# Kernel optimization log

Hardware: AMD Instinct MI355X
Metric: run time of the kernel (lower is better)

## Reference

```python
import jax, jax.numpy as jnp
import numpy as np
from jax import lax

B, T = 128, 512
V, D = 100000, 100   # word vocab, word embedding dim
H = 100              # per-direction LSTM hidden (concat -> 200)
L = 25               # number of CRF labels


def setup_inputs() -> dict:
    key = jax.random.key(0)
    ks = jax.random.split(key, 16)
    s = 0.02
    inp = {
        "tok_tensor": jax.random.randint(ks[0], (B, T), 0, V, dtype=jnp.int32),
        "tag_tensor": jax.random.randint(ks[1], (B, T), 0, L, dtype=jnp.int32),
        "lengths": jnp.full((B,), T, dtype=jnp.int32),
        "word_emb": jax.random.normal(ks[2], (V, D), jnp.float32) * s,
        # forward-direction LSTM (PyTorch gate order i,f,g,o)
        "w_ih_f": jax.random.normal(ks[3], (4 * H, D), jnp.float32) * s,
        "w_hh_f": jax.random.normal(ks[4], (4 * H, H), jnp.float32) * s,
        "b_ih_f": jax.random.normal(ks[5], (4 * H,), jnp.float32) * s,
        "b_hh_f": jax.random.normal(ks[6], (4 * H,), jnp.float32) * s,
        # backward-direction LSTM
        "w_ih_b": jax.random.normal(ks[7], (4 * H, D), jnp.float32) * s,
        "w_hh_b": jax.random.normal(ks[8], (4 * H, H), jnp.float32) * s,
        "b_ih_b": jax.random.normal(ks[9], (4 * H,), jnp.float32) * s,
        "b_hh_b": jax.random.normal(ks[10], (4 * H,), jnp.float32) * s,
        # hidden2tag linear
        "w_tag": jax.random.normal(ks[11], (L, 2 * H), jnp.float32) * s,
        "b_tag": jax.random.normal(ks[12], (L,), jnp.float32) * s,
        # CRF params
        "transitions": jax.random.normal(ks[13], (L, L), jnp.float32) * 0.1,
        "start_trans": jax.random.normal(ks[14], (L,), jnp.float32) * 0.1,
        "end_trans": jax.random.normal(ks[15], (L,), jnp.float32) * 0.1,
    }
    return inp


def _lstm(x_tbd, w_ih, w_hh, b_ih, b_hh, reverse):
    """x_tbd: [T,B,D] -> hidden states [T,B,H], aligned with input time axis."""
    Bh = x_tbd.shape[1]
    Hh = w_hh.shape[1]
    h0 = jnp.zeros((Bh, Hh), x_tbd.dtype)
    c0 = jnp.zeros((Bh, Hh), x_tbd.dtype)

    def step(carry, xt):
        h, c = carry
        gates = xt @ w_ih.T + b_ih + h @ w_hh.T + b_hh
        i, f, g, o = jnp.split(gates, 4, axis=-1)
        i = jax.nn.sigmoid(i); f = jax.nn.sigmoid(f)
        g = jnp.tanh(g); o = jax.nn.sigmoid(o)
        c = f * c + i * g
        h = o * jnp.tanh(c)
        return (h, c), h

    _, hs = lax.scan(step, (h0, c0), x_tbd, reverse=reverse)
    return hs


def _crf_nll(emissions, tags, mask, transitions, start_trans, end_trans):
    """Sum over batch of -(gold path score - log partition).
    emissions: [B,T,L], tags: [B,T] int, mask: [B,T] float (1=valid)."""
    Bb = emissions.shape[0]
    b_idx = jnp.arange(Bb)
    em_t = emissions.transpose(1, 0, 2)   # [T,B,L]
    tags_t = tags.T                       # [T,B]
    mask_t = mask.T                       # [T,B]

    # --- gold path score ---
    first_tags = tags_t[0]
    score0 = start_trans[first_tags] + em_t[0][b_idx, first_tags]

    def num_step(score, inp):
        em, tp, tc, m = inp  # emissions[t], tags[t-1], tags[t], mask[t]
        s = transitions[tp, tc] + em[b_idx, tc]
        return score + m * s, None

    gold, _ = lax.scan(num_step, score0,
                       (em_t[1:], tags_t[:-1], tags_t[1:], mask_t[1:]))
    last_idx = jnp.sum(mask, axis=1).astype(jnp.int32) - 1
    last_tags = tags[b_idx, last_idx]
    gold = gold + end_trans[last_tags]

    # --- log partition (forward algorithm) ---
    alpha0 = start_trans + em_t[0]  # [B,L]

    def part_step(alpha, inp):
        em, m = inp
        # [B,L_prev,1] + [L_prev,L_next] + [B,1,L_next]
        nxt = jax.nn.logsumexp(alpha[:, :, None] + transitions[None] + em[:, None, :], axis=1)
        alpha = jnp.where(m[:, None] > 0, nxt, alpha)
        return alpha, None

    alpha, _ = lax.scan(part_step, alpha0, (em_t[1:], mask_t[1:]))
    logZ = jax.nn.logsumexp(alpha + end_trans, axis=1)
    return jnp.sum(logZ - gold)


def reference(tok_tensor, tag_tensor, lengths,
              word_emb, w_ih_f, w_hh_f, b_ih_f, b_hh_f,
              w_ih_b, w_hh_b, b_ih_b, b_hh_b,
              w_tag, b_tag, transitions, start_trans, end_trans):
    # word embedding lookup: [B,T,D]
    tok_embs = word_emb[tok_tensor]
    x_tbd = tok_embs.transpose(1, 0, 2)  # [T,B,D]
    # BiLSTM encoder (dropout off: eval / deterministic reference)
    h_fwd = _lstm(x_tbd, w_ih_f, w_hh_f, b_ih_f, b_hh_f, reverse=False)
    h_bwd = _lstm(x_tbd, w_ih_b, w_hh_b, b_ih_b, b_hh_b, reverse=True)
    seq = jnp.concatenate([h_fwd, h_bwd], axis=-1).transpose(1, 0, 2)  # [B,T,2H]
    # hidden2tag
    emissions = jnp.einsum('btd,ld->btl', seq, w_tag) + b_tag  # [B,T,L]
    # CRF negative log-likelihood
    mask = (jnp.arange(T)[None, :] < lengths[:, None]).astype(emissions.dtype)
    return _crf_nll(emissions, tag_tensor, mask, transitions, start_trans, end_trans)
```

## Files before the change

### kernel.cpp

```cpp
#include <hip/hip_runtime.h>
#include <cstdint>
#include <cstddef>

#define BB 128
#define TT 512
#define DD 100
#define HH 100
#define NG 400
#define LL 25
#define TS 32
#define NTILE 16
#define F_LOG2E 1.44269504088896340736f
#define F_LN2   0.69314718055994530942f

typedef __decltype(__builtin_amdgcn_cvt_pkrtz(0.f, 0.f)) h2_t;
typedef _Float16 v8h __attribute__((ext_vector_type(8)));
typedef float v4f __attribute__((ext_vector_type(4)));

__device__ __forceinline__ h2_t bc_h2(unsigned int u) {
  return __builtin_bit_cast(h2_t, u);
}
__device__ __forceinline__ unsigned int pk(float x, float y) {
  return __builtin_bit_cast(unsigned int, __builtin_amdgcn_cvt_pkrtz(x, y));
}

__device__ __forceinline__ float fdot2(h2_t a, h2_t b, float c) {
#if __has_builtin(__builtin_amdgcn_fdot2)
  return __builtin_amdgcn_fdot2(a, b, c, false);
#else
  return c + (float)a[0] * (float)b[0] + (float)a[1] * (float)b[1];
#endif
}

__device__ __forceinline__ float fexp2(float x) { return __builtin_amdgcn_exp2f(x); }
__device__ __forceinline__ float flog2(float x) { return __builtin_amdgcn_logf(x); }
__device__ __forceinline__ float frcp(float x)  { return __builtin_amdgcn_rcpf(x); }

__device__ __forceinline__ float sigmoid_f(float x) {
  return frcp(1.f + fexp2(-F_LOG2E * x));
}
__device__ __forceinline__ float tanh_f(float x) {
  float e = fexp2(2.f * F_LOG2E * x);
  return 1.f - 2.f * frcp(e + 1.f);
}

template <int CTRL>
__device__ __forceinline__ float qadd(float v) {
#if __has_builtin(__builtin_amdgcn_mov_dpp)
  int m = __builtin_amdgcn_mov_dpp(__builtin_bit_cast(int, v), CTRL, 0xF, 0xF, true);
  return v + __builtin_bit_cast(float, m);
#else
  int x = (CTRL == 177) ? 1 : 2;
  return v + __shfl_xor(v, x);
#endif
}

template <int CTRL>
__device__ __forceinline__ float qperm(float v) {
#if __has_builtin(__builtin_amdgcn_mov_dpp)
  int m = __builtin_amdgcn_mov_dpp(__builtin_bit_cast(int, v), CTRL, 0xF, 0xF, true);
  return __builtin_bit_cast(float, m);
#else
  int x = (CTRL == 177) ? 1 : 2;
  return __shfl_xor(v, x);
#endif
}

__device__ __forceinline__ float rfl(float v) {
  return __builtin_bit_cast(float,
      __builtin_amdgcn_readfirstlane(__builtin_bit_cast(int, v)));
}

__device__ __forceinline__ void wave_fence() {
#if __has_builtin(__builtin_amdgcn_wave_barrier)
  __builtin_amdgcn_wave_barrier();
#endif
}

__device__ __forceinline__ void lds_barrier() {
  __builtin_amdgcn_s_waitcnt(0xC07F);
  __builtin_amdgcn_s_barrier();
}

__global__ __launch_bounds__(512, 1) void lstm_fused6(
    const int* __restrict__ tok, const float* __restrict__ emb,
    const float* __restrict__ w_ih_f, const float* __restrict__ w_ih_b,
    const float* __restrict__ b_ih_f, const float* __restrict__ b_hh_f,
    const float* __restrict__ b_ih_b, const float* __restrict__ b_hh_b,
    const float* __restrict__ w_hh_f, const float* __restrict__ w_hh_b,
    const float* __restrict__ w_tag, const float* __restrict__ b_tag,
    float* __restrict__ em_f, float* __restrict__ em_b)
{
  const int tid = threadIdx.x;
  const int b   = blockIdx.x & 127;
  const int dir = blockIdx.x >> 7;
  const float* w_hh = dir ? w_hh_b : w_hh_f;
  const float* w_ih = dir ? w_ih_b : w_ih_f;
  const float* b_ih = dir ? b_ih_b : b_ih_f;
  const float* b_hh = dir ? b_hh_b : b_hh_f;
  float* emo = dir ? em_b : em_f;

  __shared__ __align__(16) unsigned short gin_lds[TS * 400];
  __shared__ __align__(16) unsigned int xlds[TS * 68];
  __shared__ __align__(16) unsigned int hhist[TS * 68];
  __shared__ __align__(16) unsigned int hls0[56];
  __shared__ __align__(16) unsigned int hls1[56];

  const int wv   = tid >> 6;
  const int lane = tid & 63;
  const int l16  = lane & 15;
  const int quad = lane >> 4;
  const int c0b  = (25 * wv) >> 3;
  const int c1b  = (25 * (wv + 1)) >> 3;
  const int ncol = c1b - c0b;

  v8h bfr[4][4];
  int pcol[4];
#pragma unroll
  for (int ci = 0; ci < 4; ++ci) {
    const int cc = (ci < ncol) ? (c0b + ci) : c0b;
    const int n  = 16 * cc + l16;
    const float* wr = w_ih + (size_t)n * DD;
#pragma unroll
    for (int f = 0; f < 3; ++f) {
      const float* wp = wr + f * 32 + quad * 8;
      float4 va = *(const float4*)(wp);
      float4 vb = *(const float4*)(wp + 4);
      uint4 u;
      u.x = pk(va.x, va.y); u.y = pk(va.z, va.w);
      u.z = pk(vb.x, vb.y); u.w = pk(vb.z, vb.w);
      bfr[ci][f] = __builtin_bit_cast(v8h, u);
    }
    {
      uint4 u = {0u, 0u, 0u, 0u};
      if (quad == 0) {
        float4 va = *(const float4*)(wr + 96);
        u.x = pk(va.x, va.y); u.y = pk(va.z, va.w);
      }
      bfr[ci][3] = __builtin_bit_cast(v8h, u);
    }
    const int qn = (n * 41) >> 12;
    pcol[ci] = ((n - 100 * qn) << 2) + qn;
  }

  for (int i = tid; i < TS * 18; i += 512) {
    int row = i / 18;
    int d = i - row * 18;
    xlds[row * 68 + 50 + d] = 0u;
    hhist[row * 68 + 50 + d] = 0u;
  }

  const int jl = lane >> 2;
  const int gp = (lane >> 1) & 1;
  const int s2 = lane & 1;
  const int j  = 8 * jl + wv;
  const bool uact  = (jl < 12) || (jl == 12 && wv < 4);
  const int  goff  = 8 * j + 4 * gp;
  const int  hidx  = j + (j >= 50 ? 6 : 0);

  h2_t wA[25], wB[25];
  float biasA = 0.f, biasB = 0.f;
  if (uact) {
    const int g0 = 2 * gp, g1 = 2 * gp + 1;
    const float* rA = w_hh + (size_t)(g0 * 100 + j) * HH + 50 * s2;
    const float* rB = w_hh + (size_t)(g1 * 100 + j) * HH + 50 * s2;
#pragma unroll
    for (int d = 0; d < 25; ++d) {
      float2 vA = *(const float2*)(rA + 2 * d);
      float2 vB = *(const float2*)(rB + 2 * d);
      wA[d] = __builtin_amdgcn_cvt_pkrtz(vA.x, vA.y);
      wB[d] = __builtin_amdgcn_cvt_pkrtz(vB.x, vB.y);
    }
    biasA = b_ih[g0 * 100 + j] + b_hh[g0 * 100 + j];
    biasB = b_ih[g1 * 100 + j] + b_hh[g1 * 100 + j];
  }
  const float kkA = gp ? (2.f * F_LOG2E) : (-F_LOG2E);
  const float cAA = gp ? -2.f : 1.f;
  const float cBA = gp ? 1.f : 0.f;

  const int ew    = wv - 4;
  const int ecb   = ew & 1;
  const int erg   = (ew >> 1) & 1;
  const int encol = 16 * ecb + l16;
  const bool eact2 = (wv >= 4) && (encol < LL);
  v8h etag[4];
  float ebias = 0.f;
  if (wv >= 4) {
#pragma unroll
    for (int f = 0; f < 3; ++f) {
      uint4 u = {0u, 0u, 0u, 0u};
      if (eact2) {
        const float* wp = w_tag + (size_t)encol * 200 + dir * 100 + f * 32 + quad * 8;
        float4 va = *(const float4*)(wp);
        float4 vb = *(const float4*)(wp + 4);
        u.x = pk(va.x, va.y); u.y = pk(va.z, va.w);
        u.z = pk(vb.x, vb.y); u.w = pk(vb.z, vb.w);
      }
      etag[f] = __builtin_bit_cast(v8h, u);
    }
    {
      uint4 u = {0u, 0u, 0u, 0u};
      if (eact2 && quad == 0) {
        float4 va = *(const float4*)(w_tag + (size_t)encol * 200 + dir * 100 + 96);
        u.x = pk(va.x, va.y); u.y = pk(va.z, va.w);
      }
      etag[3] = __builtin_bit_cast(v8h, u);
    }
    if (eact2 && dir == 0) ebias = b_tag[encol];
  }

  if (tid < 56) { hls0[tid] = 0u; hls1[tid] = 0u; }

  const int tprow = tid / 13;
  const int tps   = tid - 13 * tprow;
  const bool tp_act = tid < 416;

  float4 xa = {0, 0, 0, 0}, xb = {0, 0, 0, 0};
  if (tp_act) {
    int ii = tprow;
    int tt = dir ? (TT - 1 - ii) : ii;
    int tk = tok[b * TT + tt];
    const float* xp = emb + (size_t)tk * DD + 8 * tps;
    xa = *(const float4*)xp;
    if (tps < 12) xb = *(const float4*)(xp + 4);
  }

  float c = 0.f;
  unsigned int gnext = 0u;

#define SD2(d, hw) { h2_t hv = bc_h2(hw);                                  \
  pA = fdot2(wA[d], hv, pA); pB = fdot2(wB[d], hv, pB); }

#define SCAN2(HRD, HWR, ROW)                                               \
  {                                                                        \
    if (uact) {                                                            \
      unsigned int gcurr = gnext;                                          \
      int nr = ((ROW) < TS - 1) ? (ROW) + 1 : TS - 1;                      \
      gnext = *(const unsigned int*)((const char*)gin_lds + nr * 800 + goff); \
      const unsigned int* hp = (HRD) + 28 * s2;                            \
      uint4 u0 = *((const uint4*)hp);                                      \
      uint4 u1 = *((const uint4*)(hp + 4));                                \
      uint4 u2 = *((const uint4*)(hp + 8));                                \
      uint4 u3 = *((const uint4*)(hp + 12));                               \
      uint4 u4 = *((const uint4*)(hp + 16));                               \
      uint4 u5 = *((const uint4*)(hp + 20));                               \
      unsigned int u6 = hp[24];                                            \
      float pA = 0.f, pB = 0.f;                                            \
      SD2(0, u0.x)  SD2(1, u0.y)  SD2(2, u0.z)  SD2(3, u0.w)               \
      SD2(4, u1.x)  SD2(5, u1.y)  SD2(6, u1.z)  SD2(7, u1.w)               \
      SD2(8, u2.x)  SD2(9, u2.y)  SD2(10, u2.z) SD2(11, u2.w)              \
      SD2(12, u3.x) SD2(13, u3.y) SD2(14, u3.z) SD2(15, u3.w)              \
      SD2(16, u4.x) SD2(17, u4.y) SD2(18, u4.z) SD2(19, u4.w)              \
      SD2(20, u5.x) SD2(21, u5.y) SD2(22, u5.z) SD2(23, u5.w)              \
      SD2(24, u6)                                                          \
      pA = qadd<177>(pA); pB = qadd<177>(pB);                              \
      h2_t gx = bc_h2(gcurr);                                              \
      float gA = pA + biasA + (float)gx[0];                                \
      float gB = pB + biasB + (float)gx[1];                                \
      float yA = fexp2(kkA * gA);                                          \
      float rA_ = frcp(1.f + yA);                                          \
      float actA = fmaf(cAA, rA_, cBA);                                    \
      float actB = sigmoid_f(gB);                                          \
      float othA = qperm<78>(actA);                                        \
      float othB = qperm<78>(actB);                                        \
      float prod = actA * othA;                                            \
      float fsel = gp ? othB : actB;                                       \
      float osel = gp ? actB : othB;                                       \
      c = fmaf(fsel, c, prod);                                             \
      float hvv = osel * tanh_f(c);                                        \
      if ((lane & 3) == 0) {                                               \
        __fp16 hh = (__fp16)hvv;                                           \
        ((__fp16*)(HWR))[hidx] = hh;                                       \
        ((__fp16*)hhist)[(ROW) * 136 + j] = hh;                            \
      }                                                                    \
    }                                                                      \
    lds_barrier();                                                         \
  }

#define EMIT_GEMM(TB)                                                      \
  {                                                                        \
    const unsigned int* hb = hhist + (erg * 16 + l16) * 68 + quad * 4;     \
    v8h ah0 = __builtin_bit_cast(v8h, *(const uint4*)(hb));                \
    v8h ah1 = __builtin_bit_cast(v8h, *(const uint4*)(hb + 16));           \
    v8h ah2 = __builtin_bit_cast(v8h, *(const uint4*)(hb + 32));           \
    v8h ah3 = __builtin_bit_cast(v8h, *(const uint4*)(hb + 48));           \
    v4f ea = {0.f, 0.f, 0.f, 0.f};                                         \
    ea = __builtin_amdgcn_mfma_f32_16x16x32_f16(ah0, etag[0], ea, 0, 0, 0);\
    ea = __builtin_amdgcn_mfma_f32_16x16x32_f16(ah1, etag[1], ea, 0, 0, 0);\
    ea = __builtin_amdgcn_mfma_f32_16x16x32_f16(ah2, etag[2], ea, 0, 0, 0);\
    ea = __builtin_amdgcn_mfma_f32_16x16x32_f16(ah3, etag[3], ea, 0, 0, 0);\
    if (eact2) {                                                           \
      const int tb = (TB) + erg * 16 + quad * 4;                           \
      _Pragma("unroll")                                                    \
      for (int r = 0; r < 4; ++r) {                                        \
        int t = dir ? (TT - 1 - (tb + r)) : (tb + r);                      \
        emo[((size_t)b * TT + t) * LL + encol] = ea[r] + ebias;            \
      }                                                                    \
    }                                                                      \
  }

  __syncthreads();

  for (int T = 0; T < NTILE; ++T) {
    if (tp_act) {
      unsigned int* xr = xlds + tprow * 68 + 4 * tps;
      if (tps < 12) {
        uint4 u;
        u.x = pk(xa.x, xa.y); u.y = pk(xa.z, xa.w);
        u.z = pk(xb.x, xb.y); u.w = pk(xb.z, xb.w);
        *(uint4*)xr = u;
      } else {
        xr[0] = pk(xa.x, xa.y);
        xr[1] = pk(xa.z, xa.w);
      }
    }
    __syncthreads();

    {
      v8h af[2][4];
#pragma unroll
      for (int rg = 0; rg < 2; ++rg)
#pragma unroll
        for (int f = 0; f < 4; ++f)
          af[rg][f] = __builtin_bit_cast(v8h,
              *(const uint4*)(xlds + (rg * 16 + l16) * 68 + f * 16 + quad * 4));

      if (tp_act && T + 1 < NTILE) {
        int ii = (T + 1) * TS + tprow;
        int tt = dir ? (TT - 1 - ii) : ii;
        int tk = tok[b * TT + tt];
        const float* xp = emb + (size_t)tk * DD + 8 * tps;
        xa = *(const float4*)xp;
        if (tps < 12) xb = *(const float4*)(xp + 4);
      }

      __fp16* gout = (__fp16*)gin_lds;
#pragma unroll
      for (int ci = 0; ci < 4; ++ci) {
        if (ci >= ncol) break;
        const int p = pcol[ci];
#pragma unroll
        for (int rg = 0; rg < 2; ++rg) {
          v4f acc = {0.f, 0.f, 0.f, 0.f};
          acc = __builtin_amdgcn_mfma_f32_16x16x32_f16(af[rg][0], bfr[ci][0], acc, 0, 0, 0);
          acc = __builtin_amdgcn_mfma_f32_16x16x32_f16(af[rg][1], bfr[ci][1], acc, 0, 0, 0);
          acc = __builtin_amdgcn_mfma_f32_16x16x32_f16(af[rg][2], bfr[ci][2], acc, 0, 0, 0);
          acc = __builtin_amdgcn_mfma_f32_16x16x32_f16(af[rg][3], bfr[ci][3], acc, 0, 0, 0);
          const int rowb = rg * 16 + quad * 4;
#pragma unroll
          for (int r = 0; r < 4; ++r)
            gout[(rowb + r) * 400 + p] = (__fp16)acc[r];
        }
      }

      if (wv >= 4 && T > 0) {
        EMIT_GEMM((T - 1) * TS)
      }
    }
    __syncthreads();
    if (uact) gnext = *(const unsigned int*)((const char*)gin_lds + goff);

    for (int it = 0; it < TS; it += 2) {
      SCAN2(hls0, hls1, it)
      SCAN2(hls1, hls0, it + 1)
    }
  }

  if (wv >= 4) {
    EMIT_GEMM((NTILE - 1) * TS)
  }
#undef EMIT_GEMM
#undef SCAN2
#undef SD2
}

#define CHN  8
#define CLEN 64
__device__ __align__(16) float g_PT[(size_t)BB * CHN * LL * 28];

__global__ __launch_bounds__(128, 2) void crf_chunks(
    const float* __restrict__ em_f, const float* __restrict__ em_b,
    const float* __restrict__ trans)
{
  const int tid = threadIdx.x;
  const int b   = blockIdx.x >> 3;
  const int c   = blockIdx.x & 7;
  const int ts  = c * CLEN;

  __shared__ __align__(16) float Al[2][LL][28];
  __shared__ __align__(16) float el[CLEN][32];

  {
    const int row  = tid >> 1;
    const int half = tid & 1;
    const int jb   = half ? 13 : 0;
    const int nj   = half ? 12 : 13;
    const float* pf = em_f + ((size_t)b * TT + ts + row) * LL;
    const float* pb = em_b + ((size_t)b * TT + ts + row) * LL;
    for (int q = 0; q < nj; ++q) {
      int jj = jb + q;
      el[row][jj] = fexp2((pf[jj] + pb[jj]) * F_LOG2E);
    }
  }

  const bool lact = tid < 125;
  const int i  = tid / 5;
  const int jg = tid - 5 * i;
  const int j0 = 5 * jg;

  float E[25][5];
  if (lact) {
#pragma unroll
    for (int k = 0; k < 25; ++k) {
      const float* tr = trans + k * 25 + j0;
#pragma unroll
      for (int u = 0; u < 5; ++u)
        E[k][u] = fexp2(tr[u] * F_LOG2E - 5.f);
    }
#pragma unroll
    for (int u = 0; u < 5; ++u)
      Al[0][i][j0 + u] = (i == j0 + u) ? 1.f : 0.f;
  }
  __syncthreads();

  int p = 0;
  const int s0 = (c == 0) ? 1 : 0;
  for (int st = s0; st < CLEN; ++st) {
    if (lact) {
      const float* ar = &Al[p][i][0];
      float4 q0 = *(const float4*)(ar);
      float4 q1 = *(const float4*)(ar + 4);
      float4 q2 = *(const float4*)(ar + 8);
      float4 q3 = *(const float4*)(ar + 12);
      float4 q4 = *(const float4*)(ar + 16);
      float4 q5 = *(const float4*)(ar + 20);
      float a24 = ar[24];
      float e0 = el[st][j0];
      float e1 = el[st][j0 + 1];
      float e2 = el[st][j0 + 2];
      float e3 = el[st][j0 + 3];
      float e4 = el[st][j0 + 4];
      float av[25] = {q0.x, q0.y, q0.z, q0.w, q1.x, q1.y, q1.z, q1.w,
                      q2.x, q2.y, q2.z, q2.w, q3.x, q3.y, q3.z, q3.w,
                      q4.x, q4.y, q4.z, q4.w, q5.x, q5.y, q5.z, q5.w, a24};
      float c0 = 0.f, c1 = 0.f, c2 = 0.f, c3 = 0.f, c4 = 0.f;
#pragma unroll
      for (int k = 0; k < 25; ++k) {
        float avk = av[k];
        c0 = fmaf(avk, E[k][0], c0);
        c1 = fmaf(avk, E[k][1], c1);
        c2 = fmaf(avk, E[k][2], c2);
        c3 = fmaf(avk, E[k][3], c3);
        c4 = fmaf(avk, E[k][4], c4);
      }
      float* wr = &Al[p ^ 1][i][j0];
      wr[0] = c0 * e0; wr[1] = c1 * e1; wr[2] = c2 * e2;
      wr[3] = c3 * e3; wr[4] = c4 * e4;
    }
    __syncthreads();
    p ^= 1;
  }

  if (lact) {
    const size_t base = ((size_t)(b * CHN + c)) * LL;
#pragma unroll
    for (int u = 0; u < 5; ++u)
      g_PT[(base + (j0 + u)) * 28 + i] = Al[p][i][j0 + u];
  }
}

__global__ __launch_bounds__(128) void crf_combine(
    const float* __restrict__ em_f, const float* __restrict__ em_b,
    const int* __restrict__ tags, const int* __restrict__ lengths,
    const float* __restrict__ trans,
    const float* __restrict__ startt, const float* __restrict__ endt,
    float* __restrict__ out)
{
  const int tid = threadIdx.x;
  const int b   = blockIdx.x;

  __shared__ __align__(16) float Vs[28];

  if (tid < 64) {
    const int lane = tid;
    const int j = (lane < LL) ? lane : 0;
    const float* ef0 = em_f + (size_t)b * TT * LL;
    const float* eb0 = em_b + (size_t)b * TT * LL;
    float v = fexp2((startt[j] + ef0[j] + eb0[j]) * F_LOG2E);
    float C = 0.f;
    for (int c = 0; c < CHN; ++c) {
      if (lane < LL) Vs[lane] = v;
      wave_fence();
      float4 s0 = *(const float4*)(Vs);
      float4 s1 = *(const float4*)(Vs + 4);
      float4 s2 = *(const float4*)(Vs + 8);
      float4 s3 = *(const float4*)(Vs + 12);
      float4 s4 = *(const float4*)(Vs + 16);
      float4 s5 = *(const float4*)(Vs + 20);
      float s24 = Vs[24];
      wave_fence();
      const float* pr = g_PT + ((size_t)(b * CHN + c) * LL + j) * 28;
      float4 p0 = *(const float4*)(pr);
      float4 p1 = *(const float4*)(pr + 4);
      float4 p2 = *(const float4*)(pr + 8);
      float4 p3 = *(const float4*)(pr + 12);
      float4 p4 = *(const float4*)(pr + 16);
      float4 p5 = *(const float4*)(pr + 20);
      float p24 = pr[24];
      float nv = s0.x * p0.x;
      nv = fmaf(s0.y, p0.y, nv); nv = fmaf(s0.z, p0.z, nv); nv = fmaf(s0.w, p0.w, nv);
      nv = fmaf(s1.x, p1.x, nv); nv = fmaf(s1.y, p1.y, nv);
      nv = fmaf(s1.z, p1.z, nv); nv = fmaf(s1.w, p1.w, nv);
      nv = fmaf(s2.x, p2.x, nv); nv = fmaf(s2.y, p2.y, nv);
      nv = fmaf(s2.z, p2.z, nv); nv = fmaf(s2.w, p2.w, nv);
      nv = fmaf(s3.x, p3.x, nv); nv = fmaf(s3.y, p3.y, nv);
      nv = fmaf(s3.z, p3.z, nv); nv = fmaf(s3.w, p3.w, nv);
      nv = fmaf(s4.x, p4.x, nv); nv = fmaf(s4.y, p4.y, nv);
      nv = fmaf(s4.z, p4.z, nv); nv = fmaf(s4.w, p4.w, nv);
      nv = fmaf(s5.x, p5.x, nv); nv = fmaf(s5.y, p5.y, nv);
      nv = fmaf(s5.z, p5.z, nv); nv = fmaf(s5.w, p5.w, nv);
      nv = fmaf(s24, p24, nv);
      float nv0 = rfl(nv);
      int k = ((__builtin_bit_cast(int, nv0) >> 23) & 255) - 127;
      k = (k > 100) ? 100 : ((k < -100) ? -100 : k);
      float scl = __builtin_bit_cast(float, (127 - k) << 23);
      v = nv * scl;
      C += (float)k;
    }
    float term = (lane < LL) ? v * fexp2(endt[j] * F_LOG2E) : 0.f;
    for (int o = 32; o > 0; o >>= 1) term += __shfl_down(term, o);
    if (lane == 0)
      atomicAdd(out, (flog2(term) + C + 5.f * 511.f) * F_LN2);
  } else {
    const int lane = tid & 63;
    const int len = lengths[b];
    float acc = 0.f;
#pragma unroll
    for (int k = 0; k < 8; ++k) {
      int t = k * 64 + lane;
      int tg = tags[b * TT + t];
      size_t ei = ((size_t)b * TT + t) * LL + tg;
      float e = em_f[ei] + em_b[ei];
      float term;
      if (t == 0) term = startt[tg] + e;
      else        term = trans[tags[b * TT + t - 1] * LL + tg] + e;
      if (t == len - 1) term += endt[tg];
      if (t < len) acc += term;
    }
    for (int o = 32; o > 0; o >>= 1) acc += __shfl_down(acc, o);
    if (lane == 0) atomicAdd(out, -acc);
  }
}

extern "C" void kernel_launch(void* const* d_in, const int* in_sizes, int n_in,
                              void* d_out, int out_size, void* d_ws, size_t ws_size,
                              hipStream_t stream) {
  const int*   tok   = (const int*)d_in[0];
  const int*   tags  = (const int*)d_in[1];
  const int*   lens  = (const int*)d_in[2];
  const float* emb   = (const float*)d_in[3];
  const float* wif   = (const float*)d_in[4];
  const float* whf   = (const float*)d_in[5];
  const float* bif   = (const float*)d_in[6];
  const float* bhf   = (const float*)d_in[7];
  const float* wib   = (const float*)d_in[8];
  const float* whb   = (const float*)d_in[9];
  const float* bib   = (const float*)d_in[10];
  const float* bhb   = (const float*)d_in[11];
  const float* wtag  = (const float*)d_in[12];
  const float* btag  = (const float*)d_in[13];
  const float* trans = (const float*)d_in[14];
  const float* st    = (const float*)d_in[15];
  const float* en    = (const float*)d_in[16];

  char* wsb = (char*)d_ws;
  float* em_f = (float*)wsb;
  float* em_b = (float*)(wsb + 6553600);

  hipMemsetAsync(d_out, 0, sizeof(float), stream);

  lstm_fused6<<<256, 512, 0, stream>>>(tok, emb, wif, wib, bif, bhf, bib, bhb,
                                       whf, whb, wtag, btag, em_f, em_b);
  crf_chunks<<<BB * CHN, 128, 0, stream>>>(em_f, em_b, trans);
  crf_combine<<<BB, 128, 0, stream>>>(em_f, em_b, tags, lens, trans, st, en,
                                      (float*)d_out);
}
```

Before: 416.9 us.

## Batch 16 sequences per block and run the LSTM recurrence on MFMA

Replaces the per-sequence LSTM block (256 blocks, fdot2 recurrence with a tiled input GEMM) with 16 blocks that each process 16 batch rows. Each step is a single MFMA GEMM over the concatenated [h, x] with fused gate activations. Hidden states go to a global fp16 buffer, and a separate emit_gemm kernel computes the emissions for both directions at once, so the CRF kernels read one summed emission array. This turns the serial recurrence into tensor-core work, but only 16 CUs are busy during the long sequential scan. It also adds an extra global round-trip for the hidden states.

```diff
diff --git a/kernel.cpp b/kernel.cpp
--- a/kernel.cpp
+++ b/kernel.cpp
@@ -6,10 +6,7 @@
 #define TT 512
 #define DD 100
 #define HH 100
-#define NG 400
 #define LL 25
-#define TS 32
-#define NTILE 16
 #define F_LOG2E 1.44269504088896340736f
 #define F_LN2   0.69314718055994530942f
 
@@ -17,19 +14,8 @@
 typedef _Float16 v8h __attribute__((ext_vector_type(8)));
 typedef float v4f __attribute__((ext_vector_type(4)));
 
-__device__ __forceinline__ h2_t bc_h2(unsigned int u) {
-  return __builtin_bit_cast(h2_t, u);
-}
 __device__ __forceinline__ unsigned int pk(float x, float y) {
   return __builtin_bit_cast(unsigned int, __builtin_amdgcn_cvt_pkrtz(x, y));
-}
-
-__device__ __forceinline__ float fdot2(h2_t a, h2_t b, float c) {
-#if __has_builtin(__builtin_amdgcn_fdot2)
-  return __builtin_amdgcn_fdot2(a, b, c, false);
-#else
-  return c + (float)a[0] * (float)b[0] + (float)a[1] * (float)b[1];
-#endif
 }
 
 __device__ __forceinline__ float fexp2(float x) { return __builtin_amdgcn_exp2f(x); }
@@ -42,28 +28,6 @@
 __device__ __forceinline__ float tanh_f(float x) {
   float e = fexp2(2.f * F_LOG2E * x);
   return 1.f - 2.f * frcp(e + 1.f);
-}
-
-template <int CTRL>
-__device__ __forceinline__ float qadd(float v) {
-#if __has_builtin(__builtin_amdgcn_mov_dpp)
-  int m = __builtin_amdgcn_mov_dpp(__builtin_bit_cast(int, v), CTRL, 0xF, 0xF, true);
-  return v + __builtin_bit_cast(float, m);
-#else
-  int x = (CTRL == 177) ? 1 : 2;
-  return v + __shfl_xor(v, x);
-#endif
-}
-
-template <int CTRL>
-__device__ __forceinline__ float qperm(float v) {
-#if __has_builtin(__builtin_amdgcn_mov_dpp)
-  int m = __builtin_amdgcn_mov_dpp(__builtin_bit_cast(int, v), CTRL, 0xF, 0xF, true);
-  return __builtin_bit_cast(float, m);
-#else
-  int x = (CTRL == 177) ? 1 : 2;
-  return __shfl_xor(v, x);
-#endif
 }
 
 __device__ __forceinline__ float rfl(float v) {
@@ -82,29 +46,28 @@
   __builtin_amdgcn_s_barrier();
 }
 
-__global__ __launch_bounds__(512, 1) void lstm_fused6(
+#define MF(a, b, c) __builtin_amdgcn_mfma_f32_16x16x32_f16(a, b, c, 0, 0, 0)
+#define LD8(base, off) __builtin_bit_cast(v8h, *(const uint4*)((base) + (off)))
+
+__device__ __align__(16) unsigned short g_h[(size_t)2 * 8 * TT * 16 * 112];
+
+__global__ __launch_bounds__(512, 1) void scan16(
     const int* __restrict__ tok, const float* __restrict__ emb,
     const float* __restrict__ w_ih_f, const float* __restrict__ w_ih_b,
+    const float* __restrict__ w_hh_f, const float* __restrict__ w_hh_b,
     const float* __restrict__ b_ih_f, const float* __restrict__ b_hh_f,
-    const float* __restrict__ b_ih_b, const float* __restrict__ b_hh_b,
-    const float* __restrict__ w_hh_f, const float* __restrict__ w_hh_b,
-    const float* __restrict__ w_tag, const float* __restrict__ b_tag,
-    float* __restrict__ em_f, float* __restrict__ em_b)
+    const float* __restrict__ b_ih_b, const float* __restrict__ b_hh_b)
 {
   const int tid = threadIdx.x;
-  const int b   = blockIdx.x & 127;
-  const int dir = blockIdx.x >> 7;
+  const int dir = blockIdx.x >> 3;
+  const int bg  = blockIdx.x & 7;
+  const int b0  = bg * 16;
   const float* w_hh = dir ? w_hh_b : w_hh_f;
   const float* w_ih = dir ? w_ih_b : w_ih_f;
   const float* b_ih = dir ? b_ih_b : b_ih_f;
   const float* b_hh = dir ? b_hh_b : b_hh_f;
-  float* emo = dir ? em_b : em_f;
-
-  __shared__ __align__(16) unsigned short gin_lds[TS * 400];
-  __shared__ __align__(16) unsigned int xlds[TS * 68];
-  __shared__ __align__(16) unsigned int hhist[TS * 68];
-  __shared__ __align__(16) unsigned int hls0[56];
-  __shared__ __align__(16) unsigned int hls1[56];
+
+  __shared__ __align__(16) unsigned short sbuf[2][16][264];
 
   const int wv   = tid >> 6;
   const int lane = tid & 63;
@@ -114,264 +77,241 @@
   const int c1b  = (25 * (wv + 1)) >> 3;
   const int ncol = c1b - c0b;
 
-  v8h bfr[4][4];
-  int pcol[4];
+  v8h wfr[4][8];
+  float bias[4][4];
 #pragma unroll
   for (int ci = 0; ci < 4; ++ci) {
-    const int cc = (ci < ncol) ? (c0b + ci) : c0b;
-    const int n  = 16 * cc + l16;
-    const float* wr = w_ih + (size_t)n * DD;
-#pragma unroll
-    for (int f = 0; f < 3; ++f) {
-      const float* wp = wr + f * 32 + quad * 8;
+    const int ct = (ci < ncol) ? (c0b + ci) : c0b;
+    const int prow = 16 * ct + l16;
+    const int jA = prow >> 2;
+    const int gA = prow & 3;
+    const float* hr = w_hh + (size_t)(gA * 100 + jA) * HH;
+    const float* ir = w_ih + (size_t)(gA * 100 + jA) * DD;
+#pragma unroll
+    for (int kc = 0; kc < 3; ++kc) {
+      const float* wp = hr + kc * 32 + quad * 8;
       float4 va = *(const float4*)(wp);
       float4 vb = *(const float4*)(wp + 4);
       uint4 u;
       u.x = pk(va.x, va.y); u.y = pk(va.z, va.w);
       u.z = pk(vb.x, vb.y); u.w = pk(vb.z, vb.w);
-      bfr[ci][f] = __builtin_bit_cast(v8h, u);
+      wfr[ci][kc] = __builtin_bit_cast(v8h, u);
     }
     {
       uint4 u = {0u, 0u, 0u, 0u};
       if (quad == 0) {
-        float4 va = *(const float4*)(wr + 96);
+        float4 va = *(const float4*)(hr + 96);
         u.x = pk(va.x, va.y); u.y = pk(va.z, va.w);
       }
-      bfr[ci][3] = __builtin_bit_cast(v8h, u);
-    }
-    const int qn = (n * 41) >> 12;
-    pcol[ci] = ((n - 100 * qn) << 2) + qn;
-  }
-
-  for (int i = tid; i < TS * 18; i += 512) {
-    int row = i / 18;
-    int d = i - row * 18;
-    xlds[row * 68 + 50 + d] = 0u;
-    hhist[row * 68 + 50 + d] = 0u;
-  }
-
-  const int jl = lane >> 2;
-  const int gp = (lane >> 1) & 1;
-  const int s2 = lane & 1;
-  const int j  = 8 * jl + wv;
-  const bool uact  = (jl < 12) || (jl == 12 && wv < 4);
-  const int  goff  = 8 * j + 4 * gp;
-  const int  hidx  = j + (j >= 50 ? 6 : 0);
-
-  h2_t wA[25], wB[25];
-  float biasA = 0.f, biasB = 0.f;
-  if (uact) {
-    const int g0 = 2 * gp, g1 = 2 * gp + 1;
-    const float* rA = w_hh + (size_t)(g0 * 100 + j) * HH + 50 * s2;
-    const float* rB = w_hh + (size_t)(g1 * 100 + j) * HH + 50 * s2;
-#pragma unroll
-    for (int d = 0; d < 25; ++d) {
-      float2 vA = *(const float2*)(rA + 2 * d);
-      float2 vB = *(const float2*)(rB + 2 * d);
-      wA[d] = __builtin_amdgcn_cvt_pkrtz(vA.x, vA.y);
-      wB[d] = __builtin_amdgcn_cvt_pkrtz(vB.x, vB.y);
-    }
-    biasA = b_ih[g0 * 100 + j] + b_hh[g0 * 100 + j];
-    biasB = b_ih[g1 * 100 + j] + b_hh[g1 * 100 + j];
-  }
-  const float kkA = gp ? (2.f * F_LOG2E) : (-F_LOG2E);
-  const float cAA = gp ? -2.f : 1.f;
-  const float cBA = gp ? 1.f : 0.f;
-
-  const int ew    = wv - 4;
-  const int ecb   = ew & 1;
-  const int erg   = (ew >> 1) & 1;
-  const int encol = 16 * ecb + l16;
-  const bool eact2 = (wv >= 4) && (encol < LL);
-  v8h etag[4];
-  float ebias = 0.f;
-  if (wv >= 4) {
-#pragma unroll
-    for (int f = 0; f < 3; ++f) {
-      uint4 u = {0u, 0u, 0u, 0u};
-      if (eact2) {
-        const float* wp = w_tag + (size_t)encol * 200 + dir * 100 + f * 32 + quad * 8;
-        float4 va = *(const float4*)(wp);
-        float4 vb = *(const float4*)(wp + 4);
-        u.x = pk(va.x, va.y); u.y = pk(va.z, va.w);
-        u.z = pk(vb.x, vb.y); u.w = pk(vb.z, vb.w);
-      }
-      etag[f] = __builtin_bit_cast(v8h, u);
+      wfr[ci][3] = __builtin_bit_cast(v8h, u);
+    }
+#pragma unroll
+    for (int kc = 0; kc < 3; ++kc) {
+      const float* wp = ir + kc * 32 + quad * 8;
+      float4 va = *(const float4*)(wp);
+      float4 vb = *(const float4*)(wp + 4);
+      uint4 u;
+      u.x = pk(va.x, va.y); u.y = pk(va.z, va.w);
+      u.z = pk(vb.x, vb.y); u.w = pk(vb.z, vb.w);
+      wfr[ci][4 + kc] = __builtin_bit_cast(v8h, u);
     }
     {
       uint4 u = {0u, 0u, 0u, 0u};
-      if (eact2 && quad == 0) {
-        float4 va = *(const float4*)(w_tag + (size_t)encol * 200 + dir * 100 + 96);
+      if (quad == 0) {
+        float4 va = *(const float4*)(ir + 96);
         u.x = pk(va.x, va.y); u.y = pk(va.z, va.w);
       }
-      etag[3] = __builtin_bit_cast(v8h, u);
-    }
-    if (eact2 && dir == 0) ebias = b_tag[encol];
-  }
-
-  if (tid < 56) { hls0[tid] = 0u; hls1[tid] = 0u; }
-
-  const int tprow = tid / 13;
-  const int tps   = tid - 13 * tprow;
-  const bool tp_act = tid < 416;
-
-  float4 xa = {0, 0, 0, 0}, xb = {0, 0, 0, 0};
-  if (tp_act) {
-    int ii = tprow;
-    int tt = dir ? (TT - 1 - ii) : ii;
-    int tk = tok[b * TT + tt];
-    const float* xp = emb + (size_t)tk * DD + 8 * tps;
-    xa = *(const float4*)xp;
-    if (tps < 12) xb = *(const float4*)(xp + 4);
-  }
-
-  float c = 0.f;
-  unsigned int gnext = 0u;
-
-#define SD2(d, hw) { h2_t hv = bc_h2(hw);                                  \
-  pA = fdot2(wA[d], hv, pA); pB = fdot2(wB[d], hv, pB); }
-
-#define SCAN2(HRD, HWR, ROW)                                               \
+      wfr[ci][7] = __builtin_bit_cast(v8h, u);
+    }
+    const int u_own = 4 * ct + quad;
+#pragma unroll
+    for (int r = 0; r < 4; ++r)
+      bias[ci][r] = b_ih[r * 100 + u_own] + b_hh[r * 100 + u_own];
+  }
+
+  const bool ldr = tid < 400;
+  const int lrow = tid / 25;
+  const int lseg = tid - 25 * lrow;
+
+  unsigned short* ghb = g_h + (size_t)(dir * 8 + bg) * TT * 16 * 112;
+
+  for (int i = tid; i < 4224; i += 512) ((unsigned int*)sbuf)[i] = 0u;
+  float4 xA = {0, 0, 0, 0}, xB = {0, 0, 0, 0};
+  if (ldr) {
+    int ta = dir ? (TT - 1) : 0;
+    int tk = tok[(b0 + lrow) * TT + ta];
+    xA = *(const float4*)(emb + (size_t)tk * DD + lseg * 4);
+  }
+  __syncthreads();
+  if (ldr) {
+    uint2 w; w.x = pk(xA.x, xA.y); w.y = pk(xA.z, xA.w);
+    *(uint2*)(&sbuf[0][lrow][128 + lseg * 4]) = w;
+    int ta1 = dir ? (TT - 2) : 1;
+    int tk1 = tok[(b0 + lrow) * TT + ta1];
+    xA = *(const float4*)(emb + (size_t)tk1 * DD + lseg * 4);
+    int ta2 = dir ? (TT - 3) : 2;
+    int tk2 = tok[(b0 + lrow) * TT + ta2];
+    xB = *(const float4*)(emb + (size_t)tk2 * DD + lseg * 4);
+  }
+  __syncthreads();
+
+  float cst[4] = {0.f, 0.f, 0.f, 0.f};
+
+#define SSTEP(T, XS)                                                        \
   {                                                                        \
-    if (uact) {                                                            \
-      unsigned int gcurr = gnext;                                          \
-      int nr = ((ROW) < TS - 1) ? (ROW) + 1 : TS - 1;                      \
-      gnext = *(const unsigned int*)((const char*)gin_lds + nr * 800 + goff); \
-      const unsigned int* hp = (HRD) + 28 * s2;                            \
-      uint4 u0 = *((const uint4*)hp);                                      \
-      uint4 u1 = *((const uint4*)(hp + 4));                                \
-      uint4 u2 = *((const uint4*)(hp + 8));                                \
-      uint4 u3 = *((const uint4*)(hp + 12));                               \
-      uint4 u4 = *((const uint4*)(hp + 16));                               \
-      uint4 u5 = *((const uint4*)(hp + 20));                               \
-      unsigned int u6 = hp[24];                                            \
-      float pA = 0.f, pB = 0.f;                                            \
-      SD2(0, u0.x)  SD2(1, u0.y)  SD2(2, u0.z)  SD2(3, u0.w)               \
-      SD2(4, u1.x)  SD2(5, u1.y)  SD2(6, u1.z)  SD2(7, u1.w)               \
-      SD2(8, u2.x)  SD2(9, u2.y)  SD2(10, u2.z) SD2(11, u2.w)              \
-      SD2(12, u3.x) SD2(13, u3.y) SD2(14, u3.z) SD2(15, u3.w)              \
-      SD2(16, u4.x) SD2(17, u4.y) SD2(18, u4.z) SD2(19, u4.w)              \
-      SD2(20, u5.x) SD2(21, u5.y) SD2(22, u5.z) SD2(23, u5.w)              \
-      SD2(24, u6)                                                          \
-      pA = qadd<177>(pA); pB = qadd<177>(pB);                              \
-      h2_t gx = bc_h2(gcurr);                                              \
-      float gA = pA + biasA + (float)gx[0];                                \
-      float gB = pB + biasB + (float)gx[1];                                \
-      float yA = fexp2(kkA * gA);                                          \
-      float rA_ = frcp(1.f + yA);                                          \
-      float actA = fmaf(cAA, rA_, cBA);                                    \
-      float actB = sigmoid_f(gB);                                          \
-      float othA = qperm<78>(actA);                                        \
-      float othB = qperm<78>(actB);                                        \
-      float prod = actA * othA;                                            \
-      float fsel = gp ? othB : actB;                                       \
-      float osel = gp ? actB : othB;                                       \
-      c = fmaf(fsel, c, prod);                                             \
-      float hvv = osel * tanh_f(c);                                        \
-      if ((lane & 3) == 0) {                                               \
-        __fp16 hh = (__fp16)hvv;                                           \
-        ((__fp16*)(HWR))[hidx] = hh;                                       \
-        ((__fp16*)hhist)[(ROW) * 136 + j] = hh;                            \
+    const int p = (T) & 1;                                                 \
+    const int ta = dir ? (TT - 1 - (T)) : (T);                             \
+    const unsigned short* bh = &sbuf[1 - p][l16][0];                       \
+    const unsigned short* bx = &sbuf[p][l16][128];                         \
+    v8h f0 = LD8(bh, 0 + quad * 8);                                        \
+    v8h f1 = LD8(bh, 32 + quad * 8);                                       \
+    v8h f2 = LD8(bh, 64 + quad * 8);                                       \
+    v8h f3 = LD8(bh, 96 + quad * 8);                                       \
+    v8h f4 = LD8(bx, 0 + quad * 8);                                        \
+    v8h f5 = LD8(bx, 32 + quad * 8);                                       \
+    v8h f6 = LD8(bx, 64 + quad * 8);                                       \
+    v8h f7 = LD8(bx, 96 + quad * 8);                                       \
+    _Pragma("unroll")                                                      \
+    for (int ci = 0; ci < 4; ++ci) {                                       \
+      if (ci >= ncol) break;                                               \
+      v4f acc = {0.f, 0.f, 0.f, 0.f};                                      \
+      acc = MF(wfr[ci][0], f0, acc);                                       \
+      acc = MF(wfr[ci][1], f1, acc);                                       \
+      acc = MF(wfr[ci][2], f2, acc);                                       \
+      acc = MF(wfr[ci][3], f3, acc);                                       \
+      acc = MF(wfr[ci][4], f4, acc);                                       \
+      acc = MF(wfr[ci][5], f5, acc);                                       \
+      acc = MF(wfr[ci][6], f6, acc);                                       \
+      acc = MF(wfr[ci][7], f7, acc);                                       \
+      float iv = sigmoid_f(acc[0] + bias[ci][0]);                          \
+      float fv = sigmoid_f(acc[1] + bias[ci][1]);                          \
+      float gv = tanh_f(acc[2] + bias[ci][2]);                             \
+      float ov = sigmoid_f(acc[3] + bias[ci][3]);                          \
+      cst[ci] = fmaf(fv, cst[ci], iv * gv);                                \
+      float hv = ov * tanh_f(cst[ci]);                                     \
+      unsigned short hh = __builtin_bit_cast(unsigned short, (__fp16)hv);  \
+      const int u_own = 4 * (c0b + ci) + quad;                             \
+      sbuf[p][l16][u_own] = hh;                                            \
+      ghb[((size_t)ta * 16 + l16) * 112 + u_own] = hh;                     \
+    }                                                                      \
+    if (ldr) {                                                             \
+      if ((T) + 1 < TT) {                                                  \
+        uint2 w; w.x = pk(XS.x, XS.y); w.y = pk(XS.z, XS.w);               \
+        *(uint2*)(&sbuf[1 - p][lrow][128 + lseg * 4]) = w;                 \
       }                                                                    \
+      int s = ((T) + 3 < TT) ? (T) + 3 : (TT - 1);                         \
+      int tas = dir ? (TT - 1 - s) : s;                                    \
+      int tk = tok[(b0 + lrow) * TT + tas];                                \
+      XS = *(const float4*)(emb + (size_t)tk * DD + lseg * 4);             \
     }                                                                      \
     lds_barrier();                                                         \
   }
 
-#define EMIT_GEMM(TB)                                                      \
-  {                                                                        \
-    const unsigned int* hb = hhist + (erg * 16 + l16) * 68 + quad * 4;     \
-    v8h ah0 = __builtin_bit_cast(v8h, *(const uint4*)(hb));                \
-    v8h ah1 = __builtin_bit_cast(v8h, *(const uint4*)(hb + 16));           \
-    v8h ah2 = __builtin_bit_cast(v8h, *(const uint4*)(hb + 32));           \
-    v8h ah3 = __builtin_bit_cast(v8h, *(const uint4*)(hb + 48));           \
-    v4f ea = {0.f, 0.f, 0.f, 0.f};                                         \
-    ea = __builtin_amdgcn_mfma_f32_16x16x32_f16(ah0, etag[0], ea, 0, 0, 0);\
-    ea = __builtin_amdgcn_mfma_f32_16x16x32_f16(ah1, etag[1], ea, 0, 0, 0);\
-    ea = __builtin_amdgcn_mfma_f32_16x16x32_f16(ah2, etag[2], ea, 0, 0, 0);\
-    ea = __builtin_amdgcn_mfma_f32_16x16x32_f16(ah3, etag[3], ea, 0, 0, 0);\
-    if (eact2) {                                                           \
-      const int tb = (TB) + erg * 16 + quad * 4;                           \
-      _Pragma("unroll")                                                    \
-      for (int r = 0; r < 4; ++r) {                                        \
-        int t = dir ? (TT - 1 - (tb + r)) : (tb + r);                      \
-        emo[((size_t)b * TT + t) * LL + encol] = ea[r] + ebias;            \
-      }                                                                    \
-    }                                                                      \
-  }
-
+  for (int t2 = 0; t2 < TT; t2 += 2) {
+    SSTEP(t2, xA)
+    SSTEP(t2 + 1, xB)
+  }
+#undef SSTEP
+}
+
+__global__ __launch_bounds__(512, 1) void emit_gemm(
+    const float* __restrict__ w_tag, const float* __restrict__ b_tag,
+    float* __restrict__ em)
+{
+  const int tid = threadIdx.x;
+  const int bg  = blockIdx.x & 7;
+  const int tc  = blockIdx.x >> 3;
+  const int t0  = tc * 8;
+  const int b0  = bg * 16;
+
+  __shared__ __align__(16) unsigned short hb[8][2][16][136];
+
+  const int wv   = tid >> 6;
+  const int lane = tid & 63;
+  const int l16  = lane & 15;
+  const int quad = lane >> 4;
+
+  v8h wfr[2][2][4];
+  float bo[2][4];
+#pragma unroll
+  for (int lt = 0; lt < 2; ++lt) {
+    const int label = lt * 16 + l16;
+    const bool valid = label < LL;
+#pragma unroll
+    for (int d = 0; d < 2; ++d) {
+      const float* wr = w_tag + (size_t)(valid ? label : 0) * 200 + d * 100;
+#pragma unroll
+      for (int kc = 0; kc < 3; ++kc) {
+        uint4 u = {0u, 0u, 0u, 0u};
+        if (valid) {
+          const float* wp = wr + kc * 32 + quad * 8;
+          float4 va = *(const float4*)(wp);
+          float4 vb = *(const float4*)(wp + 4);
+          u.x = pk(va.x, va.y); u.y = pk(va.z, va.w);
+          u.z = pk(vb.x, vb.y); u.w = pk(vb.z, vb.w);
+        }
+        wfr[lt][d][kc] = __builtin_bit_cast(v8h, u);
+      }
+      {
+        uint4 u = {0u, 0u, 0u, 0u};
+        if (valid && quad == 0) {
+          float4 va = *(const float4*)(wr + 96);
+          u.x = pk(va.x, va.y); u.y = pk(va.z, va.w);
+        }
+        wfr[lt][d][3] = __builtin_bit_cast(v8h, u);
+      }
+    }
+#pragma unroll
+    for (int r = 0; r < 4; ++r) {
+      int lab = lt * 16 + 4 * quad + r;
+      bo[lt][r] = (lab < LL) ? b_tag[lab] : 0.f;
+    }
+  }
+
+  for (int i = tid; i < 256 * 18; i += 512) {
+    int r = i / 18, k = i - 18 * r;
+    *(unsigned int*)((char*)hb + r * 272 + 200 + k * 4) = 0u;
+  }
   __syncthreads();
 
-  for (int T = 0; T < NTILE; ++T) {
-    if (tp_act) {
-      unsigned int* xr = xlds + tprow * 68 + 4 * tps;
-      if (tps < 12) {
-        uint4 u;
-        u.x = pk(xa.x, xa.y); u.y = pk(xa.z, xa.w);
-        u.z = pk(xb.x, xb.y); u.w = pk(xb.z, xb.w);
-        *(uint4*)xr = u;
-      } else {
-        xr[0] = pk(xa.x, xa.y);
-        xr[1] = pk(xa.z, xa.w);
-      }
-    }
-    __syncthreads();
-
-    {
-      v8h af[2][4];
-#pragma unroll
-      for (int rg = 0; rg < 2; ++rg)
-#pragma unroll
-        for (int f = 0; f < 4; ++f)
-          af[rg][f] = __builtin_bit_cast(v8h,
-              *(const uint4*)(xlds + (rg * 16 + l16) * 68 + f * 16 + quad * 4));
-
-      if (tp_act && T + 1 < NTILE) {
-        int ii = (T + 1) * TS + tprow;
-        int tt = dir ? (TT - 1 - ii) : ii;
-        int tk = tok[b * TT + tt];
-        const float* xp = emb + (size_t)tk * DD + 8 * tps;
-        xa = *(const float4*)xp;
-        if (tps < 12) xb = *(const float4*)(xp + 4);
-      }
-
-      __fp16* gout = (__fp16*)gin_lds;
-#pragma unroll
-      for (int ci = 0; ci < 4; ++ci) {
-        if (ci >= ncol) break;
-        const int p = pcol[ci];
-#pragma unroll
-        for (int rg = 0; rg < 2; ++rg) {
-          v4f acc = {0.f, 0.f, 0.f, 0.f};
-          acc = __builtin_amdgcn_mfma_f32_16x16x32_f16(af[rg][0], bfr[ci][0], acc, 0, 0, 0);
-          acc = __builtin_amdgcn_mfma_f32_16x16x32_f16(af[rg][1], bfr[ci][1], acc, 0, 0, 0);
-          acc = __builtin_amdgcn_mfma_f32_16x16x32_f16(af[rg][2], bfr[ci][2], acc, 0, 0, 0);
-          acc = __builtin_amdgcn_mfma_f32_16x16x32_f16(af[rg][3], bfr[ci][3], acc, 0, 0, 0);
-          const int rowb = rg * 16 + quad * 4;
-#pragma unroll
-          for (int r = 0; r < 4; ++r)
-            gout[(rowb + r) * 400 + p] = (__fp16)acc[r];
-        }
-      }
-
-      if (wv >= 4 && T > 0) {
-        EMIT_GEMM((T - 1) * TS)
-      }
-    }
-    __syncthreads();
-    if (uact) gnext = *(const unsigned int*)((const char*)gin_lds + goff);
-
-    for (int it = 0; it < TS; it += 2) {
-      SCAN2(hls0, hls1, it)
-      SCAN2(hls1, hls0, it + 1)
-    }
-  }
-
-  if (wv >= 4) {
-    EMIT_GEMM((NTILE - 1) * TS)
-  }
-#undef EMIT_GEMM
-#undef SCAN2
-#undef SD2
+  for (int i = tid; i < 256 * 13; i += 512) {
+    int row = i / 13, cp = i - 13 * row;
+    int tloc = row >> 5, d = (row >> 4) & 1, b = row & 15;
+    const char* src = (const char*)(g_h +
+        (size_t)(d * 8 + bg) * TT * 16 * 112 +
+        ((size_t)(t0 + tloc) * 16 + b) * 112);
+    char* dst = (char*)hb + row * 272;
+    if (cp < 12)
+      *(uint4*)(dst + cp * 16) = *(const uint4*)(src + cp * 16);
+    else
+      *(uint2*)(dst + 192) = *(const uint2*)(src + 192);
+  }
+  __syncthreads();
+
+  v8h fh[2][4];
+#pragma unroll
+  for (int d = 0; d < 2; ++d)
+#pragma unroll
+    for (int kc = 0; kc < 4; ++kc)
+      fh[d][kc] = LD8(&hb[wv][d][l16][0], kc * 32 + quad * 8);
+
+#pragma unroll
+  for (int lt = 0; lt < 2; ++lt) {
+    v4f acc = {0.f, 0.f, 0.f, 0.f};
+#pragma unroll
+    for (int d = 0; d < 2; ++d) {
+      acc = MF(wfr[lt][d][0], fh[d][0], acc);
+      acc = MF(wfr[lt][d][1], fh[d][1], acc);
+      acc = MF(wfr[lt][d][2], fh[d][2], acc);
+      acc = MF(wfr[lt][d][3], fh[d][3], acc);
+    }
+#pragma unroll
+    for (int r = 0; r < 4; ++r) {
+      int lab = lt * 16 + 4 * quad + r;
+      if (lab < LL)
+        em[((size_t)(b0 + l16) * TT + (t0 + wv)) * LL + lab] = acc[r] + bo[lt][r];
+    }
+  }
 }
 
 #define CHN  8
@@ -379,8 +319,7 @@
 __device__ __align__(16) float g_PT[(size_t)BB * CHN * LL * 28];
 
 __global__ __launch_bounds__(128, 2) void crf_chunks(
-    const float* __restrict__ em_f, const float* __restrict__ em_b,
-    const float* __restrict__ trans)
+    const float* __restrict__ em, const float* __restrict__ trans)
 {
   const int tid = threadIdx.x;
   const int b   = blockIdx.x >> 3;
@@ -395,11 +334,10 @@
     const int half = tid & 1;
     const int jb   = half ? 13 : 0;
     const int nj   = half ? 12 : 13;
-    const float* pf = em_f + ((size_t)b * TT + ts + row) * LL;
-    const float* pb = em_b + ((size_t)b * TT + ts + row) * LL;
+    const float* pe = em + ((size_t)b * TT + ts + row) * LL;
     for (int q = 0; q < nj; ++q) {
       int jj = jb + q;
-      el[row][jj] = fexp2((pf[jj] + pb[jj]) * F_LOG2E);
+      el[row][jj] = fexp2(pe[jj] * F_LOG2E);
     }
   }
 
@@ -470,7 +408,7 @@
 }
 
 __global__ __launch_bounds__(128) void crf_combine(
-    const float* __restrict__ em_f, const float* __restrict__ em_b,
+    const float* __restrict__ em,
     const int* __restrict__ tags, const int* __restrict__ lengths,
     const float* __restrict__ trans,
     const float* __restrict__ startt, const float* __restrict__ endt,
@@ -484,9 +422,8 @@
   if (tid < 64) {
     const int lane = tid;
     const int j = (lane < LL) ? lane : 0;
-    const float* ef0 = em_f + (size_t)b * TT * LL;
-    const float* eb0 = em_b + (size_t)b * TT * LL;
-    float v = fexp2((startt[j] + ef0[j] + eb0[j]) * F_LOG2E);
+    const float* e0p = em + (size_t)b * TT * LL;
+    float v = fexp2((startt[j] + e0p[j]) * F_LOG2E);
     float C = 0.f;
     for (int c = 0; c < CHN; ++c) {
       if (lane < LL) Vs[lane] = v;
@@ -540,7 +477,7 @@
       int t = k * 64 + lane;
       int tg = tags[b * TT + t];
       size_t ei = ((size_t)b * TT + t) * LL + tg;
-      float e = em_f[ei] + em_b[ei];
+      float e = em[ei];
       float term;
       if (t == 0) term = startt[tg] + e;
       else        term = trans[tags[b * TT + t - 1] * LL + tg] + e;
@@ -573,15 +510,14 @@
   const float* st    = (const float*)d_in[15];
   const float* en    = (const float*)d_in[16];
 
-  char* wsb = (char*)d_ws;
-  float* em_f = (float*)wsb;
-  float* em_b = (float*)(wsb + 6553600);
+  float* em = (float*)d_ws;
 
   hipMemsetAsync(d_out, 0, sizeof(float), stream);
 
-  lstm_fused6<<<256, 512, 0, stream>>>(tok, emb, wif, wib, bif, bhf, bib, bhb,
-                                       whf, whb, wtag, btag, em_f, em_b);
-  crf_chunks<<<BB * CHN, 128, 0, stream>>>(em_f, em_b, trans);
-  crf_combine<<<BB, 128, 0, stream>>>(em_f, em_b, tags, lens, trans, st, en,
+  scan16<<<16, 512, 0, stream>>>(tok, emb, wif, wib, whf, whb,
+                                 bif, bhf, bib, bhb);
+  emit_gemm<<<512, 512, 0, stream>>>(wtag, btag, em);
+  crf_chunks<<<BB * CHN, 128, 0, stream>>>(em, trans);
+  crf_combine<<<BB, 128, 0, stream>>>(em, tags, lens, trans, st, en,
                                       (float*)d_out);
 }
```

New measurement: 848.8 us. 104% more time.
